# Optimization experiments

Hardware: AMD Instinct MI355X
Metric: run time of the kernel (lower is better)

The kernel has to match this reference:

```python
import jax, jax.numpy as jnp
import numpy as np
from jax import lax

# ---- static config (matches init_kwargs) ----
ORDER = 1
NPTS = ORDER + 1            # 2
JUNC_K = 300
LINE_K = 5000
NMS_SIZE = 3
JUNC_THRESH = 0.008
EPS = 1e-5
B, C, H, W = 4, 256, 160, 160
HID = C // 4                # 64
OUT_CH = [1, 1, 2, 1, 2, 4]  # lmap,jmap,joff,cmap,coff,lvec
NHEADS = len(OUT_CH)
MAXO = max(OUT_CH)          # pad conv2 out-channels to 4 per head
# channel-select indices from padded (NHEADS*MAXO) grouped-conv output
SEL = np.array([h * MAXO + c for h, k in enumerate(OUT_CH) for c in range(k)])
# lvec channel permutation from original forward (identity for order=1)
PERM = np.arange(OUT_CH[-1]).reshape(-1, 2, 2)
PERM[:, 1] = PERM[::-1, 1]
PERM = PERM.reshape(-1)


def setup_inputs() -> dict:
    key = jax.random.key(0)
    ks = jax.random.split(key, 9)
    features = jax.random.normal(ks[0], (B, C, H, W), jnp.float32)
    w1 = jax.random.normal(ks[1], (NHEADS * HID, C, 3, 3), jnp.float32) / np.sqrt(C * 9)
    b1 = 0.01 * jax.random.normal(ks[2], (NHEADS * HID,), jnp.float32)
    gamma = 1.0 + 0.1 * jax.random.normal(ks[3], (NHEADS * HID,), jnp.float32)
    beta = 0.01 * jax.random.normal(ks[4], (NHEADS * HID,), jnp.float32)
    mean = 0.1 * jax.random.normal(ks[5], (NHEADS * HID,), jnp.float32)
    var = jax.random.uniform(ks[6], (NHEADS * HID,), jnp.float32, 0.5, 1.5)
    w2 = jax.random.normal(ks[7], (NHEADS * MAXO, HID, 3, 3), jnp.float32) / np.sqrt(HID * 9)
    b2 = 0.01 * jax.random.normal(ks[8], (NHEADS * MAXO,), jnp.float32)
    return dict(features=features, w1=w1, b1=b1, gamma=gamma, beta=beta,
                mean=mean, var=var, w2=w2, b2=b2)


def _conv(x, w, b, groups=1):
    y = lax.conv_general_dilated(x, w, (1, 1), 'SAME',
                                 dimension_numbers=('NCHW', 'OIHW', 'NCHW'),
                                 feature_group_count=groups)
    return y + b[None, :, None, None]


def _nms(hm):  # hm: (1,H,W) -> suppress non-peaks
    mx = lax.reduce_window(hm, -jnp.inf, lax.max, (1, NMS_SIZE, NMS_SIZE),
                           (1, 1, 1), [(0, 0), (1, 1), (1, 1)])
    return jnp.where(hm == mx, hm, 0.0)


def _post(jm, joff, cm, coff, lv):
    """Per-sample postprocess. jm,cm:(1,H,W) joff,coff:(2,H,W) lv:(4,H,W).
    Returns (pts:(LINE_K,2,2) padded lines, mask:(LINE_K,) validity)."""
    # junctions: NMS + top-K + thresh mask + offset gather
    sj, ij = lax.top_k(_nms(jm).reshape(-1), JUNC_K)
    valid_j = sj >= JUNC_THRESH
    xy = jnp.stack([ij % W, ij // W], -1).astype(jm.dtype)
    junc = xy + joff.reshape(2, -1).T[ij] + 0.5
    junc = jnp.stack([jnp.clip(junc[:, 0], 0.0, W - 1e-4),
                      jnp.clip(junc[:, 1], 0.0, H - 1e-4)], -1)
    # lines: top-K centers + vector field gather (thresh=0 -> always full K)
    sc, ic = lax.top_k(cm.reshape(-1), LINE_K)
    cxy = jnp.stack([ic % W, ic // W], -1).astype(cm.dtype)
    center = cxy + coff.reshape(2, -1).T[ic] + 0.5
    lvr = lv.reshape(NPTS // 2 * 2, 2, -1).transpose(2, 0, 1)  # (HW,2,2)
    loi = center[:, None] + lvr[ic]                            # (L,2,2)
    loi = jnp.stack([jnp.clip(loi[..., 0], 0.0, W - 1e-4),
                     jnp.clip(loi[..., 1], 0.0, H - 1e-4)], -1)
    # pairwise squared-distance argmin of each endpoint to junctions
    d1 = ((loi[:, None, 0] - junc[None]) ** 2).sum(-1)
    d2 = ((loi[:, None, -1] - junc[None]) ** 2).sum(-1)
    big = jnp.asarray(1e18, d1.dtype)
    i1 = jnp.argmin(jnp.where(valid_j[None], d1, big), axis=-1)
    i2 = jnp.argmin(jnp.where(valid_j[None], d2, big), axis=-1)
    imin = jnp.minimum(i1, i2)
    imax = jnp.maximum(i1, i2)
    keep = imin != imax
    # unique (imin,imax) pairs via sorted-key dedup (matches torch.unique order)
    BIGK = JUNC_K * JUNC_K
    keyv = jnp.where(keep, imin * JUNC_K + imax, BIGK)
    sk = jnp.sort(keyv)
    first = jnp.concatenate([jnp.ones((1,), bool), sk[1:] != sk[:-1]]) & (sk < BIGK)
    a = jnp.where(first, sk // JUNC_K, 0)
    b = jnp.where(first, sk % JUNC_K, 0)
    pts = jnp.stack([junc[a], junc[b]], axis=1)  # (L,2,2)
    swap = pts[:, 0, 1] > pts[:, 1, 1]
    pts = jnp.where(swap[:, None, None], pts[:, ::-1], pts)
    return pts, first


def _maps(features, w1, b1, gamma, beta, mean, var, w2, b2):
    y = _conv(features, w1, b1)
    y = (y - mean[None, :, None, None]) * gamma[None, :, None, None] * \
        lax.rsqrt(var + EPS)[None, :, None, None] + beta[None, :, None, None]
    y = jax.nn.relu(y)
    y = _conv(y, w2, b2, groups=NHEADS)        # (B, NHEADS*MAXO, H, W)
    m = y[:, SEL]                              # (B, 11, H, W)
    lmap = jax.nn.sigmoid(m[:, 0:1])
    jmap = jax.nn.sigmoid(m[:, 1:2])
    joff = m[:, 2:4]
    cmap = jax.nn.sigmoid(m[:, 4:5])
    coff = m[:, 5:7]
    lvec = m[:, 7:][:, PERM]
    return lmap, jmap, joff, cmap, coff, lvec


def reference(features, w1, b1, gamma, beta, mean, var, w2, b2):
    lmap, jmap, joff, cmap, coff, lvec = _maps(features, w1, b1, gamma, beta,
                                               mean, var, w2, b2)
    loi, mask = jax.vmap(_post)(jmap, joff, cmap, coff, lvec)
    return lmap, jmap, joff, cmap, coff, lvec, loi, mask


if __name__ == '__main__':
    out = reference(**setup_inputs())
    for o in out:
        print(o.shape, o.dtype)
```

## Files before the change

### kernel.cpp

```cpp
#include <hip/hip_runtime.h>
#include <math.h>

#define IMG   160
#define HWSZ  25600
#define NB    4
#define CIN   256
#define COUT1 384
#define BIGK  90000

#define OFF_LMAP 0
#define OFF_JMAP 102400
#define OFF_JOFF 204800
#define OFF_CMAP 409600
#define OFF_COFF 512000
#define OFF_LVEC 716800
#define OFF_LOI  1126400
#define OFF_MASK 1206400

static const size_t WS_Y1    = 0;
static const size_t WS_JSORT = (size_t)NB * COUT1 * HWSZ * 4;
static const size_t WS_CSORT = WS_JSORT + (size_t)NB * 32768 * 8;
static const size_t WS_JUNC  = WS_CSORT + (size_t)NB * 32768 * 8;
static const size_t WS_JVAL  = WS_JUNC + (size_t)NB * 300 * 2 * 4;
static const size_t WS_LKEY  = WS_JVAL + (size_t)NB * 300 * 4;
static const size_t WS_WPK   = WS_LKEY + (size_t)NB * 8192 * 4;
static const size_t WS_AFTER_WPK = WS_WPK + (size_t)12 * 8 * 9 * 32 * 64 * 2;
static const size_t WS_BNS   = WS_AFTER_WPK;
static const size_t WS_JM    = WS_BNS + 384 * 4;
static const size_t WS_CM    = WS_JM + (size_t)NB * 300 * 8;
static const size_t WS_FPK   = WS_CM + (size_t)NB * 5000 * 8;
static const size_t WS_NEED_MIN = WS_FPK;
static const size_t WS_NEED_PK = WS_FPK + (size_t)NB * 8 * 162 * 162 * 128;

typedef unsigned long long u64;
typedef __attribute__((ext_vector_type(8))) short short8;
typedef __attribute__((ext_vector_type(4))) float f32x4;
typedef __attribute__((ext_vector_type(4))) int int4v;

union frag_u { short8 s8; u64 u[2]; int4v v; };

__device__ __forceinline__ float clip_coord(float v) {
    return fminf(fmaxf(v, 0.0f), 159.9999f);
}
__device__ __forceinline__ float sigmoidf(float v) {
    return 1.0f / (1.0f + expf(-v));
}
__device__ __forceinline__ unsigned short f2bf(float f) {
    unsigned u = __float_as_uint(f);
    return (unsigned short)((u + 0x7FFFu + ((u >> 16) & 1u)) >> 16);
}
__device__ __forceinline__ float bf2f(unsigned short h) {
    return __uint_as_float((unsigned)h << 16);
}

__device__ __forceinline__ void async_copy16(void* lds, const void* g) {
    __builtin_amdgcn_global_load_lds(
        (const __attribute__((address_space(1))) unsigned int*)g,
        (__attribute__((address_space(3))) unsigned int*)lds, 16, 0, 0);
}


__global__ __launch_bounds__(256) void prep_kernel(
    const float* __restrict__ w1, short* __restrict__ wpk,
    const float* __restrict__ gamma, const float* __restrict__ var,
    float* __restrict__ bns,
    const float* __restrict__ feat, short* __restrict__ fpk) {
    const int blk = blockIdx.x;
    const int tid = threadIdx.x;
    if (blk < 6912) {
        int e = blk * 256 + tid;
        int row = e >> 6, sp = e & 63;
        int ocl = row & 31;
        int tap = (row >> 5) % 9;
        int icc = (row / 288) & 7;
        int octile = row / 2304;
        int p16 = sp >> 3, j = sp & 7;
        int l16 = p16 ^ (ocl & 7);
        int ql = l16 * 8 + j;
        int term = ql >> 5, icl = ql & 31;
        int oc = octile * 32 + ocl, ic = icc * 32 + icl;
        float a = w1[((size_t)oc * CIN + ic) * 9 + tap];
        unsigned short hi = f2bf(a);
        wpk[e] = (term == 0) ? (short)hi : (short)f2bf(a - bf2f(hi));
        return;
    }
    if (blk == 6912) {
        for (int i = tid; i < COUT1; i += 256)
            bns[i] = gamma[i] / sqrtf(var[i] + 1e-5f);
        return;
    }
    const int c4  = (tid >> 4) & 3;
    const int r0  = (tid & 15) | (((tid >> 6) & 3) << 4);
    const int rest = (blk - 6913) * 64 + r0;
    const int px = rest % 162;
    const int t2 = rest / 162;
    const int py = t2 % 162;
    const int bi = t2 / 162;
    const int s  = (2 * py + px) & 7;
    const int gy = py - 1, gx = px - 1;
    const bool valid = ((unsigned)gy < (unsigned)IMG) && ((unsigned)gx < (unsigned)IMG);
    const float* fs = feat + (size_t)(bi * 32 + c4 * 8) * HWSZ
                           + (valid ? gy * IMG + gx : 0);
    unsigned hi4[4], lo4[4];
#pragma unroll
    for (int j2 = 0; j2 < 4; ++j2) {
        float va = valid ? fs[(size_t)(2 * j2) * HWSZ]     : 0.0f;
        float vb = valid ? fs[(size_t)(2 * j2 + 1) * HWSZ] : 0.0f;
        unsigned short ha = f2bf(va), hb = f2bf(vb);
        unsigned short la = f2bf(va - bf2f(ha)), lb = f2bf(vb - bf2f(hb));
        hi4[j2] = (unsigned)ha | ((unsigned)hb << 16);
        lo4[j2] = (unsigned)la | ((unsigned)lb << 16);
    }
    const int p0 = c4 ^ s;
    const int p1 = (c4 | 4) ^ s;
    int4v* base = (int4v*)(fpk + (size_t)rest * 64);
    base[p0] = (int4v){ (int)hi4[0], (int)hi4[1], (int)hi4[2], (int)hi4[3] };
    base[p1] = (int4v){ (int)lo4[0], (int)lo4[1], (int)lo4[2], (int)lo4[3] };
}

__global__ __launch_bounds__(512, 2) void conv1_mfma_pk(
    const short* __restrict__ fpk, const short* __restrict__ wpk,
    const float* __restrict__ b1, const float* __restrict__ bns,
    const float* __restrict__ beta, const float* __restrict__ mean,
    float* __restrict__ y1) {
    const int bid   = blockIdx.x;
    const int slot  = bid >> 3;
    const int tile  = (bid & 7) + ((slot / 12) << 3);
    const int octile = slot - (slot / 12) * 12;
    const int bb = tile / 50, tt = tile % 50;
    const int ty = (tt / 5) * 16, tx = (tt % 5) * 32;
    const int oc0 = octile * 32;
    const int tid  = threadIdx.x;
    const int wid  = tid >> 6;
    const int wr   = wid >> 1;
    const int wc   = wid & 1;
    const int lane = tid & 63;
    const int quad = lane >> 4;
    const int l15  = lane & 15;
    const int wbase = tid & ~63;

    __shared__ __align__(16) short Alds[2][288 * 64];
    __shared__ __align__(16) short Blds[612 * 64];

    int aoff[2];
#pragma unroll
    for (int t = 0; t < 2; ++t)
        aoff[t] = l15 * 128 + ((((t << 2) | quad) ^ (l15 & 7)) << 4);

    f32x4 acc[2][4];
#pragma unroll
    for (int mi = 0; mi < 2; ++mi)
#pragma unroll
        for (int nj = 0; nj < 4; ++nj) acc[mi][nj] = (f32x4){0.f, 0.f, 0.f, 0.f};

    const char* asrc0 = (const char*)wpk + (size_t)(octile * 8) * 36864;

    int boff[10];
#pragma unroll
    for (int it = 0; it < 10; ++it) {
        int k = it * 512 + tid;
        int hy = (int)((unsigned)k / 272u);
        int r  = k - hy * 272;
        boff[it] = hy * (162 * 128) + r * 16;
    }
    const char* bsrc0 = (const char*)fpk
        + (((size_t)(bb * 8) * 162 + ty) * 162 + tx) * 128;
    const size_t bstride = (size_t)162 * 162 * 128;

    {
        char* ad = (char*)&Alds[0][0];
#pragma unroll
        for (int i = 0; i < 4; ++i)
            async_copy16(ad + (size_t)(i * 512 + wbase) * 16,
                         asrc0 + (size_t)(i * 512 + tid) * 16);
        if (tid < 256)
            async_copy16(ad + (size_t)(2048 + wbase) * 16,
                         asrc0 + (size_t)(2048 + tid) * 16);
#pragma unroll
        for (int it = 0; it < 9; ++it)
            async_copy16((char*)Blds + (size_t)(it * 512 + wbase) * 16,
                         bsrc0 + boff[it]);
        if (tid < 288) {
            const int4v vv = *(const int4v*)(bsrc0 + boff[9]);
            *(int4v*)((char*)Blds + (size_t)(4608 + tid) * 16) = vv;
        }
    }
    __syncthreads();

    int4v pvB[10];
#pragma unroll 1
    for (int icc = 0; icc < 8; ++icc) {
        const int cur = icc & 1;
        const char* Ab = (const char*)&Alds[cur][0];

        if (icc < 7) {
            const char* as = asrc0 + (size_t)(icc + 1) * 36864;
            char* ad = (char*)&Alds[cur ^ 1][0];
#pragma unroll
            for (int i = 0; i < 4; ++i)
                async_copy16(ad + (size_t)(i * 512 + wbase) * 16,
                             as + (size_t)(i * 512 + tid) * 16);
            if (tid < 256)
                async_copy16(ad + (size_t)(2048 + wbase) * 16,
                             as + (size_t)(2048 + tid) * 16);
            const char* bs = bsrc0 + (size_t)(icc + 1) * bstride;
#pragma unroll
            for (int it = 0; it < 9; ++it)
                pvB[it] = *(const int4v*)(bs + boff[it]);
            if (tid < 288) pvB[9] = *(const int4v*)(bs + boff[9]);
        }

#pragma unroll
        for (int sx = 0; sx < 3; ++sx) {
            frag_u Bf[2][6];
#pragma unroll
            for (int t = 0; t < 2; ++t)
#pragma unroll
                for (int rr = 0; rr < 6; ++rr) {
                    int pos = (wr * 4 + rr) * 34 + (wc * 16 + l15 + sx);
                    const char* bp = (const char*)Blds + (size_t)pos * 128
                        + ((((t << 2) | quad) ^ (pos & 7)) << 4);
                    Bf[t][rr].v = *(const int4v*)bp;
                }
#pragma unroll
            for (int sy = 0; sy < 3; ++sy) {
                const int tap = sy * 3 + sx;
                frag_u Af[2][2];
#pragma unroll
                for (int t = 0; t < 2; ++t)
#pragma unroll
                    for (int mi = 0; mi < 2; ++mi) {
                        const char* ap = Ab
                            + (size_t)(tap * 32 + mi * 16) * 128 + aoff[t];
                        Af[t][mi].v = *(const int4v*)ap;
                    }
#pragma unroll
                for (int mi = 0; mi < 2; ++mi)
#pragma unroll
                    for (int nj = 0; nj < 4; ++nj) {
                        acc[mi][nj] = __builtin_amdgcn_mfma_f32_16x16x32_bf16(
                            Af[0][mi].s8, Bf[0][nj + sy].s8, acc[mi][nj], 0, 0, 0);
                        acc[mi][nj] = __builtin_amdgcn_mfma_f32_16x16x32_bf16(
                            Af[0][mi].s8, Bf[1][nj + sy].s8, acc[mi][nj], 0, 0, 0);
                        acc[mi][nj] = __builtin_amdgcn_mfma_f32_16x16x32_bf16(
                            Af[1][mi].s8, Bf[0][nj + sy].s8, acc[mi][nj], 0, 0, 0);
                    }
            }
        }

        if (icc < 7) {
            __syncthreads();
#pragma unroll
            for (int it = 0; it < 9; ++it)
                *(int4v*)((char*)Blds + (size_t)(it * 512 + tid) * 16) = pvB[it];
            if (tid < 288)
                *(int4v*)((char*)Blds + (size_t)(4608 + tid) * 16) = pvB[9];
            __syncthreads();
        }
    }

#pragma unroll
    for (int nj = 0; nj < 4; ++nj) {
        const int gy = ty + wr * 4 + nj, gx = tx + wc * 16 + l15;
#pragma unroll
        for (int mi = 0; mi < 2; ++mi)
#pragma unroll
            for (int r = 0; r < 4; ++r) {
                const int oc = oc0 + mi * 16 + quad * 4 + r;
                float v = acc[mi][nj][r] + b1[oc];
                v = (v - mean[oc]) * bns[oc] + beta[oc];
                y1[((size_t)(bb * COUT1 + oc)) * HWSZ + gy * IMG + gx] = fmaxf(v, 0.0f);
            }
    }
}


__global__ void wpack_kernel(const float* __restrict__ w1, short* __restrict__ wpk) {
    int e = blockIdx.x * 256 + threadIdx.x;
    int row = e >> 6, sp = e & 63;
    int ocl = row & 31;
    int tap = (row >> 5) % 9;
    int icc = (row / 288) & 7;
    int octile = row / 2304;
    int s = (sp >> 2) ^ (ocl & 15);
    int ql = s * 4 + (sp & 3);
    int term = ql >> 5, icl = ql & 31;
    int oc = octile * 32 + ocl, ic = icc * 32 + icl;
    float a = w1[((size_t)oc * CIN + ic) * 9 + tap];
    unsigned short hi = f2bf(a);
    wpk[e] = (term == 0) ? (short)hi : (short)f2bf(a - bf2f(hi));
}

__global__ __launch_bounds__(256, 2) void conv1_mfma(
    const float* __restrict__ feat, const short* __restrict__ wpk,
    const float* __restrict__ b1, const float* __restrict__ gamma,
    const float* __restrict__ beta, const float* __restrict__ mean,
    const float* __restrict__ var, float* __restrict__ y1) {
    const int bid   = blockIdx.x;
    const int slot  = bid >> 3;
    const int tile  = (bid & 7) + ((slot / 12) << 3);
    const int octile = slot - (slot / 12) * 12;
    const int bb = tile / 100, tt = tile % 100;
    const int ty = (tt / 10) * 16, tx = (tt % 10) * 16;
    const int oc0 = octile * 32;
    const int tid  = threadIdx.x;
    const int w    = tid >> 6;
    const int lane = tid & 63;
    const int quad = lane >> 4;
    const int l15  = lane & 15;

    __shared__ short Alds[288 * 64];
    __shared__ short Blds[324 * 68];

    int aoff[2][2];
#pragma unroll
    for (int t = 0; t < 2; ++t)
#pragma unroll
        for (int h = 0; h < 2; ++h)
            aoff[t][h] = l15 * 128 + (((t * 8 + quad * 2 + h) ^ l15) * 8);

    f32x4 acc[2][4];
#pragma unroll
    for (int mi = 0; mi < 2; ++mi)
#pragma unroll
        for (int nj = 0; nj < 4; ++nj) acc[mi][nj] = (f32x4){0.f, 0.f, 0.f, 0.f};

    const int4v* asrc_base = (const int4v*)wpk + (size_t)(octile * 8) * 2304;
    unsigned* Bd = (unsigned*)Blds;

    float pv0[21], pv1[21];

#pragma unroll
    for (int ii = 0; ii < 21; ++ii) {
        int i = tid + ii * 256;
        if (i < 5184) {
            int icp = i / 324, hp = i - icp * 324;
            int hy = hp / 18, hx = hp - hy * 18;
            int gy = ty + hy - 1, gx = tx + hx - 1;
            bool valid = ((unsigned)gy < IMG) && ((unsigned)gx < IMG);
            const float* fs = feat + ((size_t)(bb * CIN + icp * 2)) * HWSZ
                                   + (valid ? (gy * IMG + gx) : 0);
            pv0[ii] = valid ? fs[0]    : 0.0f;
            pv1[ii] = valid ? fs[HWSZ] : 0.0f;
        }
    }

#pragma unroll 1
    for (int icc = 0; icc < 8; ++icc) {
        __syncthreads();
        {
            const int4v* asrc = asrc_base + (size_t)icc * 2304;
            int4v* adst = (int4v*)Alds;
#pragma unroll
            for (int i = 0; i < 9; ++i)
                adst[tid + i * 256] = asrc[tid + i * 256];
        }
#pragma unroll
        for (int ii = 0; ii < 21; ++ii) {
            int i = tid + ii * 256;
            if (i < 5184) {
                int icp = i / 324, hp = i - icp * 324;
                float v0 = pv0[ii], v1 = pv1[ii];
                unsigned short h0 = f2bf(v0), h1 = f2bf(v1);
                unsigned short m0 = f2bf(v0 - bf2f(h0)), m1 = f2bf(v1 - bf2f(h1));
                Bd[hp * 34 + icp]      = (unsigned)h0 | ((unsigned)h1 << 16);
                Bd[hp * 34 + 16 + icp] = (unsigned)m0 | ((unsigned)m1 << 16);
            }
        }
        __syncthreads();

        if (icc < 7) {
#pragma unroll
            for (int ii = 0; ii < 21; ++ii) {
                int i = tid + ii * 256;
                if (i < 5184) {
                    int icp = i / 324, hp = i - icp * 324;
                    int hy = hp / 18, hx = hp - hy * 18;
                    int gy = ty + hy - 1, gx = tx + hx - 1;
                    bool valid = ((unsigned)gy < IMG) && ((unsigned)gx < IMG);
                    const float* fs = feat
                        + ((size_t)(bb * CIN + (icc + 1) * 32 + icp * 2)) * HWSZ
                        + (valid ? (gy * IMG + gx) : 0);
                    pv0[ii] = valid ? fs[0]    : 0.0f;
                    pv1[ii] = valid ? fs[HWSZ] : 0.0f;
                }
            }
        }

#pragma unroll
        for (int tap = 0; tap < 9; ++tap) {
            const int sy = tap / 3, sx = tap % 3;
            frag_u Af[2][2], Bf[2][4];
#pragma unroll
            for (int t = 0; t < 2; ++t) {
#pragma unroll
                for (int mi = 0; mi < 2; ++mi) {
                    const char* base = (const char*)Alds + (tap * 32 + mi * 16) * 128;
                    Af[t][mi].u[0] = *(const u64*)(base + aoff[t][0]);
                    Af[t][mi].u[1] = *(const u64*)(base + aoff[t][1]);
                }
#pragma unroll
                for (int nj = 0; nj < 4; ++nj) {
                    int pos = (w * 4 + nj + sy) * 18 + (l15 + sx);
                    const short* bp = &Blds[pos * 68 + t * 32 + quad * 8];
                    Bf[t][nj].u[0] = *(const u64*)bp;
                    Bf[t][nj].u[1] = *(const u64*)(bp + 4);
                }
            }
#pragma unroll
            for (int mi = 0; mi < 2; ++mi)
#pragma unroll
                for (int nj = 0; nj < 4; ++nj) {
                    acc[mi][nj] = __builtin_amdgcn_mfma_f32_16x16x32_bf16(
                        Af[0][mi].s8, Bf[0][nj].s8, acc[mi][nj], 0, 0, 0);
                    acc[mi][nj] = __builtin_amdgcn_mfma_f32_16x16x32_bf16(
                        Af[0][mi].s8, Bf[1][nj].s8, acc[mi][nj], 0, 0, 0);
                    acc[mi][nj] = __builtin_amdgcn_mfma_f32_16x16x32_bf16(
                        Af[1][mi].s8, Bf[0][nj].s8, acc[mi][nj], 0, 0, 0);
                    acc[mi][nj] = __builtin_amdgcn_mfma_f32_16x16x32_bf16(
                        Af[1][mi].s8, Bf[1][nj].s8, acc[mi][nj], 0, 0, 0);
                }
        }
    }

#pragma unroll
    for (int nj = 0; nj < 4; ++nj) {
        const int gy = ty + w * 4 + nj, gx = tx + l15;
#pragma unroll
        for (int mi = 0; mi < 2; ++mi)
#pragma unroll
            for (int r = 0; r < 4; ++r) {
                const int oc = oc0 + mi * 16 + quad * 4 + r;
                float v = acc[mi][nj][r] + b1[oc];
                v = (v - mean[oc]) * (gamma[oc] / sqrtf(var[oc] + 1e-5f)) + beta[oc];
                y1[((size_t)(bb * COUT1 + oc)) * HWSZ + gy * IMG + gx] = fmaxf(v, 0.0f);
            }
    }
}


__global__ __launch_bounds__(256, 2) void conv2_kernel(
    const float* __restrict__ y1, const float* __restrict__ w2,
    const float* __restrict__ b2, float* __restrict__ out) {
    const int KH[6]   = {1, 1, 2, 1, 2, 4};
    const int REG[6]  = {OFF_LMAP, OFF_JMAP, OFF_JOFF, OFF_CMAP, OFF_COFF, OFF_LVEC};
    const int SIGF[6] = {1, 1, 0, 1, 0, 0};

    const int bz = blockIdx.z;
    const int b  = bz / 6;
    const int h  = bz % 6;
    const int k  = KH[h];
    const int tx = blockIdx.x * 32, ty = blockIdx.y * 16;
    const int lx = threadIdx.x, ly = threadIdx.y;
    const int tid = ly * 16 + lx;

    __shared__ float tin[16][18][40];
    float* const tinf = &tin[0][0][0];
    float accv[4][2] = {{0.f,0.f},{0.f,0.f},{0.f,0.f},{0.f,0.f}};

    const float* yb = y1 + ((size_t)(b * COUT1 + h * 64)) * HWSZ;

    bool sok[3], sval[3];
    int  soff[3], sidx[3];
#pragma unroll
    for (int j = 0; j < 3; ++j) {
        int idx = tid + j * 256;
        sok[j] = (idx < 612);
        int r = idx / 34, col = idx - r * 34;
        int gy = ty - 1 + r, gx = tx - 1 + col;
        sval[j] = sok[j] && ((unsigned)gy < (unsigned)IMG) && ((unsigned)gx < (unsigned)IMG);
        soff[j] = sval[j] ? (gy * IMG + gx) : 0;
        sidx[j] = r * 40 + col;
    }

    for (int ic0 = 0; ic0 < 64; ic0 += 16) {
        __syncthreads();
#pragma unroll
        for (int j = 0; j < 3; ++j) {
            if (sok[j]) {
                const float* yp = yb + (size_t)ic0 * HWSZ + soff[j];
                float* tp = tinf + sidx[j];
#pragma unroll 4
                for (int c = 0; c < 16; ++c)
                    tp[c * 720] = sval[j] ? yp[(size_t)c * HWSZ] : 0.0f;
            }
        }
        __syncthreads();

        const float* tb = tinf + ly * 40 + 2 * lx;
#pragma unroll 2
        for (int c = 0; c < 16; ++c) {
            const float* tc = tb + c * 720;
            float n[3][4];
#pragma unroll
            for (int r = 0; r < 3; ++r) {
                float2 u = *(const float2*)(tc + r * 40);
                float2 v = *(const float2*)(tc + r * 40 + 2);
                n[r][0] = u.x; n[r][1] = u.y; n[r][2] = v.x; n[r][3] = v.y;
            }
#pragma unroll
            for (int o = 0; o < 4; ++o) {
                if (o < k) {
                    const float* wp = w2 + ((size_t)((h * 4 + o) * 64 + (ic0 + c))) * 9;
                    float a0 = accv[o][0], a1 = accv[o][1];
#pragma unroll
                    for (int r = 0; r < 3; ++r) {
                        float w0 = wp[3*r], w1 = wp[3*r+1], w2v = wp[3*r+2];
                        a0 = fmaf(n[r][0], w0, a0);
                        a1 = fmaf(n[r][1], w0, a1);
                        a0 = fmaf(n[r][1], w1, a0);
                        a1 = fmaf(n[r][2], w1, a1);
                        a0 = fmaf(n[r][2], w2v, a0);
                        a1 = fmaf(n[r][3], w2v, a1);
                    }
                    accv[o][0] = a0; accv[o][1] = a1;
                }
            }
        }
    }

    const int p = (ty + ly) * IMG + tx + 2 * lx;
#pragma unroll
    for (int o = 0; o < 4; ++o) {
        if (o < k) {
            float v0 = accv[o][0] + b2[h * 4 + o];
            float v1 = accv[o][1] + b2[h * 4 + o];
            if (SIGF[h]) { v0 = sigmoidf(v0); v1 = sigmoidf(v1); }
            size_t base = (size_t)REG[h] + ((size_t)(b * k + o)) * HWSZ + p;
            out[base]     = v0;
            out[base + 1] = v1;
        }
    }
}

#define SK64(i) ((i) + ((i) >> 4))
__global__ __launch_bounds__(1024) void sortnms_kernel(
    const float* __restrict__ out, u64* __restrict__ buf) {
    __shared__ u64 s[8192 + 512];
    const int bid = blockIdx.x;
    const int arr = bid >> 2, chunk = bid & 3;
    const bool isj = (arr < 4);
    const int b = arr & 3;
    const float* mp = out + (isj ? OFF_JMAP : OFF_CMAP) + (size_t)b * HWSZ;

    for (int i = threadIdx.x; i < 8192; i += 1024) {
        int p = chunk * 8192 + i;
        u64 key = 0ull;
        if (p < HWSZ) {
            float v = mp[p];
            float nv = v;
            if (isj) {
                const int x = p % IMG, y = p / IMG;
                float mx = v;
#pragma unroll
                for (int dy = -1; dy <= 1; ++dy)
#pragma unroll
                    for (int dx = -1; dx <= 1; ++dx) {
                        int nx = x + dx, ny = y + dy;
                        if (nx >= 0 && nx < IMG && ny >= 0 && ny < IMG)
                            mx = fmaxf(mx, mp[ny * IMG + nx]);
                    }
                nv = (v == mx) ? v : 0.0f;
            }
            key = ((u64)__float_as_uint(nv) << 32)
                | (u64)(0xFFFFFFFFu - (unsigned)p);
        }
        s[SK64(i)] = key;
    }
    for (int k = 2; k <= 8192; k <<= 1)
        for (int j = k >> 1; j > 0; j >>= 1) {
            __syncthreads();
            for (int t = threadIdx.x; t < 4096; t += 1024) {
                int i = ((t & ~(j - 1)) << 1) | (t & (j - 1));
                int l = i | j;
                bool desc = ((i & k) == 0);
                u64 x = s[SK64(i)], y = s[SK64(l)];
                if (desc ? (x < y) : (x > y)) { s[SK64(i)] = y; s[SK64(l)] = x; }
            }
        }
    __syncthreads();
    const size_t base = (size_t)bid * 8192;
    for (int i = threadIdx.x; i < 8192; i += 1024) buf[base + i] = s[SK64(i)];
}

__device__ __forceinline__ int count_gt_desc(const u64* __restrict__ a, u64 e) {
    int cnt = 0;
#pragma unroll
    for (int st = 8192; st > 0; st >>= 1)
        if (cnt + st <= 8192 && a[cnt + st - 1] > e) cnt += st;
    return cnt;
}

__global__ void merge_topk_kernel(const u64* __restrict__ jsort,
                                  const u64* __restrict__ csort,
                                  u64* __restrict__ jm, u64* __restrict__ cm) {
    const int b = blockIdx.y;
    int t = blockIdx.x * 256 + threadIdx.x;
    const u64* src; u64* dst; int K, chunk, pos;
    if (t < 1200) {
        src = jsort + (size_t)b * 32768; dst = jm + (size_t)b * 300;
        K = 300; chunk = t / 300; pos = t - chunk * 300;
    } else {
        t -= 1200;
        if (t >= 20000) return;
        src = csort + (size_t)b * 32768; dst = cm + (size_t)b * 5000;
        K = 5000; chunk = t / 5000; pos = t - chunk * 5000;
    }
    u64 e = src[chunk * 8192 + pos];
    int rank = pos;
#pragma unroll
    for (int c = 0; c < 4; ++c)
        if (c != chunk) rank += count_gt_desc(src + c * 8192, e);
    if (rank < K) dst[rank] = e;
}

__global__ __launch_bounds__(1024) void sort32_lds(int* __restrict__ buf) {
    __shared__ int s[8192];
    int* a = buf + (size_t)blockIdx.x * 8192;
    for (int i = threadIdx.x; i < 8192; i += 1024) s[i] = a[i];
    for (int k = 2; k <= 8192; k <<= 1)
        for (int j = k >> 1; j > 0; j >>= 1) {
            __syncthreads();
            for (int t = threadIdx.x; t < 4096; t += 1024) {
                int i = ((t & ~(j - 1)) << 1) | (t & (j - 1));
                int l = i | j;
                bool asc = ((i & k) == 0);
                int x = s[i], y = s[l];
                if (asc ? (x > y) : (x < y)) { s[i] = y; s[l] = x; }
            }
        }
    __syncthreads();
    for (int i = threadIdx.x; i < 8192; i += 1024) a[i] = s[i];
}

__global__ void lines_kernel(const u64* __restrict__ cmk,
                             const u64* __restrict__ jmk,
                             const float* __restrict__ out,
                             int* __restrict__ lkeys) {
    const int b = blockIdx.y;
    const int t = blockIdx.x * 256 + threadIdx.x;

    __shared__ float jx[300], jy[300];
    __shared__ int jv[300];
    {
        const float* j0 = out + OFF_JOFF + (size_t)(b * 2) * HWSZ;
        const float* j1 = j0 + HWSZ;
        for (int i = threadIdx.x; i < 300; i += 256) {
            u64 key = jmk[(size_t)b * 300 + i];
            float score  = __uint_as_float((unsigned)(key >> 32));
            unsigned idx = 0xFFFFFFFFu - (unsigned)(key & 0xFFFFFFFFull);
            jx[i] = clip_coord((float)(idx % IMG) + j0[idx] + 0.5f);
            jy[i] = clip_coord((float)(idx / IMG) + j1[idx] + 0.5f);
            jv[i] = (score >= 0.008f) ? 1 : 0;
        }
    }
    __syncthreads();

    if (t >= 8192) return;
    if (t >= 5000) { lkeys[b * 8192 + t] = 0x7FFFFFFF; return; }

    u64 key = cmk[(size_t)b * 5000 + t];
    unsigned idx = 0xFFFFFFFFu - (unsigned)(key & 0xFFFFFFFFull);
    const float* c0 = out + OFF_COFF + (size_t)(b * 2) * HWSZ;
    const float* c1 = c0 + HWSZ;
    const float* lv = out + OFF_LVEC + (size_t)(b * 4) * HWSZ;

    float cx = (float)(idx % IMG) + c0[idx] + 0.5f;
    float cy = (float)(idx / IMG) + c1[idx] + 0.5f;
    float e0x = clip_coord(cx + lv[idx]);
    float e0y = clip_coord(cy + lv[HWSZ + idx]);
    float e1x = clip_coord(cx + lv[2 * HWSZ + idx]);
    float e1y = clip_coord(cy + lv[3 * HWSZ + idx]);

    float m1 = 1e18f, m2 = 1e18f;
    int i1 = 0, i2 = 0;
    for (int j = 0; j < 300; ++j) {
        if (jv[j]) {
            float dx = e0x - jx[j], dy = e0y - jy[j];
            float d = dx * dx + dy * dy;
            if (d < m1) { m1 = d; i1 = j; }
            dx = e1x - jx[j]; dy = e1y - jy[j];
            d = dx * dx + dy * dy;
            if (d < m2) { m2 = d; i2 = j; }
        }
    }
    int imin = min(i1, i2), imax = max(i1, i2);
    lkeys[b * 8192 + t] = (i1 != i2) ? (imin * 300 + imax) : BIGK;
}

__global__ void finalize_kernel(const int* __restrict__ lkeys,
                                const u64* __restrict__ jmk,
                                float* __restrict__ out) {
    const int b = blockIdx.y;
    const int t = blockIdx.x * 256 + threadIdx.x;
    if (t >= 5000) return;
    const int* lk = lkeys + b * 8192;
    int sk = lk[t];
    bool first = ((t == 0) || (sk != lk[t - 1])) && (sk < BIGK);
    int a  = first ? sk / 300 : 0;
    int bb = first ? sk % 300 : 0;
    const float* j0 = out + OFF_JOFF + (size_t)(b * 2) * HWSZ;
    const float* j1 = j0 + HWSZ;
    u64 ka = jmk[(size_t)b * 300 + a];
    u64 kb = jmk[(size_t)b * 300 + bb];
    unsigned ia = 0xFFFFFFFFu - (unsigned)(ka & 0xFFFFFFFFull);
    unsigned ib = 0xFFFFFFFFu - (unsigned)(kb & 0xFFFFFFFFull);
    float p0x = clip_coord((float)(ia % IMG) + j0[ia] + 0.5f);
    float p0y = clip_coord((float)(ia / IMG) + j1[ia] + 0.5f);
    float p1x = clip_coord((float)(ib % IMG) + j0[ib] + 0.5f);
    float p1y = clip_coord((float)(ib / IMG) + j1[ib] + 0.5f);
    if (p0y > p1y) {
        float tx = p0x; p0x = p1x; p1x = tx;
        float ty = p0y; p0y = p1y; p1y = ty;
    }
    size_t base = OFF_LOI + (size_t)(b * 5000 + t) * 4;
    out[base]     = p0x;
    out[base + 1] = p0y;
    out[base + 2] = p1x;
    out[base + 3] = p1y;
    out[OFF_MASK + b * 5000 + t] = first ? 1.0f : 0.0f;
}

extern "C" void kernel_launch(void* const* d_in, const int* in_sizes, int n_in,
                              void* d_out, int out_size, void* d_ws, size_t ws_size,
                              hipStream_t stream) {
    const float* feat  = (const float*)d_in[0];
    const float* w1    = (const float*)d_in[1];
    const float* b1    = (const float*)d_in[2];
    const float* gamma = (const float*)d_in[3];
    const float* beta  = (const float*)d_in[4];
    const float* mean  = (const float*)d_in[5];
    const float* var   = (const float*)d_in[6];
    const float* w2    = (const float*)d_in[7];
    const float* b2    = (const float*)d_in[8];
    float* out = (float*)d_out;
    char*  ws  = (char*)d_ws;

    if (ws_size < WS_NEED_MIN) return;

    float* y1 = (float*)(ws + WS_Y1);
    u64* jsort = (u64*)(ws + WS_JSORT);
    int* lkeys  = (int*)(ws + WS_LKEY);
    u64* csort = (u64*)(ws + WS_CSORT);
    short* wpk = (short*)(ws + WS_WPK);
    float* bns = (float*)(ws + WS_BNS);
    u64* jm    = (u64*)(ws + WS_JM);
    u64* cm    = (u64*)(ws + WS_CM);
    short* fpk = (short*)(ws + WS_FPK);

    if (ws_size >= WS_NEED_PK) {
        prep_kernel<<<dim3(20035), dim3(256), 0, stream>>>(
            w1, wpk, gamma, var, bns, feat, fpk);
        conv1_mfma_pk<<<dim3(2400), dim3(512), 0, stream>>>(
            fpk, wpk, b1, bns, beta, mean, y1);
    } else {
        wpack_kernel<<<dim3(6912), dim3(256), 0, stream>>>(w1, wpk);
        conv1_mfma<<<dim3(4800), dim3(256), 0, stream>>>(
            feat, wpk, b1, gamma, beta, mean, var, y1);
    }

    conv2_kernel<<<dim3(5, 10, NB * 6), dim3(16, 16), 0, stream>>>(y1, w2, b2, out);

    sortnms_kernel<<<dim3(32), dim3(1024), 0, stream>>>(out, jsort);

    merge_topk_kernel<<<dim3(83, NB), dim3(256), 0, stream>>>(jsort, csort, jm, cm);

    lines_kernel<<<dim3(32, NB), dim3(256), 0, stream>>>(cm, jm, out, lkeys);

    sort32_lds<<<dim3(NB), dim3(1024), 0, stream>>>(lkeys);

    finalize_kernel<<<dim3(20, NB), dim3(256), 0, stream>>>(lkeys, jm, out);
}
```

Baseline: 1.006 ms.

## Shrink conv1 tiles to 256 threads with single-buffered LDS, fuse sort+finalize

After: 953.2 us (median of 2 runs). 5.2% less time.

```diff
diff --git a/kernel.cpp b/kernel.cpp
--- a/kernel.cpp
+++ b/kernel.cpp
@@ -118,7 +118,7 @@
     base[p1] = (int4v){ (int)lo4[0], (int)lo4[1], (int)lo4[2], (int)lo4[3] };
 }
 
-__global__ __launch_bounds__(512, 2) void conv1_mfma_pk(
+__global__ __launch_bounds__(256, 2) void conv1_mfma_pk(
     const short* __restrict__ fpk, const short* __restrict__ wpk,
     const float* __restrict__ b1, const float* __restrict__ bns,
     const float* __restrict__ beta, const float* __restrict__ mean,
@@ -127,20 +127,18 @@
     const int slot  = bid >> 3;
     const int tile  = (bid & 7) + ((slot / 12) << 3);
     const int octile = slot - (slot / 12) * 12;
-    const int bb = tile / 50, tt = tile % 50;
-    const int ty = (tt / 5) * 16, tx = (tt % 5) * 32;
+    const int bb = tile / 100, tt = tile % 100;
+    const int ty = (tt / 10) * 16, tx = (tt % 10) * 16;
     const int oc0 = octile * 32;
     const int tid  = threadIdx.x;
-    const int wid  = tid >> 6;
-    const int wr   = wid >> 1;
-    const int wc   = wid & 1;
+    const int w    = tid >> 6;
     const int lane = tid & 63;
     const int quad = lane >> 4;
     const int l15  = lane & 15;
-    const int wbase = tid & ~63;
-
-    __shared__ __align__(16) short Alds[2][288 * 64];
-    __shared__ __align__(16) short Blds[612 * 64];
+    const int wbase = tid & 192;
+
+    __shared__ __align__(16) short Alds[288 * 64];
+    __shared__ __align__(16) short Blds[324 * 64];
 
     int aoff[2];
 #pragma unroll
@@ -155,60 +153,36 @@
 
     const char* asrc0 = (const char*)wpk + (size_t)(octile * 8) * 36864;
 
-    int boff[10];
-#pragma unroll
-    for (int it = 0; it < 10; ++it) {
-        int k = it * 512 + tid;
-        int hy = (int)((unsigned)k / 272u);
-        int r  = k - hy * 272;
-        boff[it] = hy * (162 * 128) + r * 16;
-    }
-    const char* bsrc0 = (const char*)fpk
-        + (((size_t)(bb * 8) * 162 + ty) * 162 + tx) * 128;
-    const size_t bstride = (size_t)162 * 162 * 128;
-
-    {
-        char* ad = (char*)&Alds[0][0];
-#pragma unroll
-        for (int i = 0; i < 4; ++i)
-            async_copy16(ad + (size_t)(i * 512 + wbase) * 16,
-                         asrc0 + (size_t)(i * 512 + tid) * 16);
-        if (tid < 256)
-            async_copy16(ad + (size_t)(2048 + wbase) * 16,
-                         asrc0 + (size_t)(2048 + tid) * 16);
-#pragma unroll
-        for (int it = 0; it < 9; ++it)
-            async_copy16((char*)Blds + (size_t)(it * 512 + wbase) * 16,
-                         bsrc0 + boff[it]);
-        if (tid < 288) {
-            const int4v vv = *(const int4v*)(bsrc0 + boff[9]);
-            *(int4v*)((char*)Blds + (size_t)(4608 + tid) * 16) = vv;
-        }
-    }
-    __syncthreads();
-
-    int4v pvB[10];
 #pragma unroll 1
     for (int icc = 0; icc < 8; ++icc) {
-        const int cur = icc & 1;
-        const char* Ab = (const char*)&Alds[cur][0];
-
-        if (icc < 7) {
-            const char* as = asrc0 + (size_t)(icc + 1) * 36864;
-            char* ad = (char*)&Alds[cur ^ 1][0];
-#pragma unroll
-            for (int i = 0; i < 4; ++i)
-                async_copy16(ad + (size_t)(i * 512 + wbase) * 16,
-                             as + (size_t)(i * 512 + tid) * 16);
-            if (tid < 256)
-                async_copy16(ad + (size_t)(2048 + wbase) * 16,
-                             as + (size_t)(2048 + tid) * 16);
-            const char* bs = bsrc0 + (size_t)(icc + 1) * bstride;
-#pragma unroll
-            for (int it = 0; it < 9; ++it)
-                pvB[it] = *(const int4v*)(bs + boff[it]);
-            if (tid < 288) pvB[9] = *(const int4v*)(bs + boff[9]);
-        }
+        __syncthreads();
+        {
+            const char* asrc = asrc0 + (size_t)icc * 36864;
+#pragma unroll
+            for (int i = 0; i < 9; ++i) {
+                int k = i * 256 + tid;
+                async_copy16((char*)Alds + (size_t)(i * 256 + wbase) * 16,
+                             asrc + (size_t)k * 16);
+            }
+        }
+        {
+            const char* bsrc = (const char*)fpk
+                + (((size_t)(bb * 8 + icc) * 162 + ty) * 162 + tx) * 128;
+#pragma unroll
+            for (int it = 0; it < 10; ++it) {
+                int k = it * 256 + tid;
+                int hy = (int)((unsigned)k / 144u);
+                int r  = k - hy * 144;
+                async_copy16((char*)Blds + (size_t)(it * 256 + wbase) * 16,
+                             bsrc + (size_t)hy * (162 * 128) + (size_t)r * 16);
+            }
+            if (tid < 32) {
+                const int4v vv = *(const int4v*)(bsrc + (size_t)17 * (162 * 128)
+                                                 + (size_t)(112 + tid) * 16);
+                *(int4v*)((char*)Blds + (size_t)(2560 + tid) * 16) = vv;
+            }
+        }
+        __syncthreads();
 
 #pragma unroll
         for (int sx = 0; sx < 3; ++sx) {
@@ -217,7 +191,7 @@
             for (int t = 0; t < 2; ++t)
 #pragma unroll
                 for (int rr = 0; rr < 6; ++rr) {
-                    int pos = (wr * 4 + rr) * 34 + (wc * 16 + l15 + sx);
+                    int pos = (w * 4 + rr) * 18 + (l15 + sx);
                     const char* bp = (const char*)Blds + (size_t)pos * 128
                         + ((((t << 2) | quad) ^ (pos & 7)) << 4);
                     Bf[t][rr].v = *(const int4v*)bp;
@@ -230,7 +204,7 @@
                 for (int t = 0; t < 2; ++t)
 #pragma unroll
                     for (int mi = 0; mi < 2; ++mi) {
-                        const char* ap = Ab
+                        const char* ap = (const char*)Alds
                             + (size_t)(tap * 32 + mi * 16) * 128 + aoff[t];
                         Af[t][mi].v = *(const int4v*)ap;
                     }
@@ -247,21 +221,11 @@
                     }
             }
         }
-
-        if (icc < 7) {
-            __syncthreads();
-#pragma unroll
-            for (int it = 0; it < 9; ++it)
-                *(int4v*)((char*)Blds + (size_t)(it * 512 + tid) * 16) = pvB[it];
-            if (tid < 288)
-                *(int4v*)((char*)Blds + (size_t)(4608 + tid) * 16) = pvB[9];
-            __syncthreads();
-        }
     }
 
 #pragma unroll
     for (int nj = 0; nj < 4; ++nj) {
-        const int gy = ty + wr * 4 + nj, gx = tx + wc * 16 + l15;
+        const int gy = ty + w * 4 + nj, gx = tx + l15;
 #pragma unroll
         for (int mi = 0; mi < 2; ++mi)
 #pragma unroll
@@ -614,25 +578,6 @@
     if (rank < K) dst[rank] = e;
 }
 
-__global__ __launch_bounds__(1024) void sort32_lds(int* __restrict__ buf) {
-    __shared__ int s[8192];
-    int* a = buf + (size_t)blockIdx.x * 8192;
-    for (int i = threadIdx.x; i < 8192; i += 1024) s[i] = a[i];
-    for (int k = 2; k <= 8192; k <<= 1)
-        for (int j = k >> 1; j > 0; j >>= 1) {
-            __syncthreads();
-            for (int t = threadIdx.x; t < 4096; t += 1024) {
-                int i = ((t & ~(j - 1)) << 1) | (t & (j - 1));
-                int l = i | j;
-                bool asc = ((i & k) == 0);
-                int x = s[i], y = s[l];
-                if (asc ? (x > y) : (x < y)) { s[i] = y; s[l] = x; }
-            }
-        }
-    __syncthreads();
-    for (int i = threadIdx.x; i < 8192; i += 1024) a[i] = s[i];
-}
-
 __global__ void lines_kernel(const u64* __restrict__ cmk,
                              const u64* __restrict__ jmk,
                              const float* __restrict__ out,
@@ -688,37 +633,52 @@
     lkeys[b * 8192 + t] = (i1 != i2) ? (imin * 300 + imax) : BIGK;
 }
 
-__global__ void finalize_kernel(const int* __restrict__ lkeys,
-                                const u64* __restrict__ jmk,
-                                float* __restrict__ out) {
-    const int b = blockIdx.y;
-    const int t = blockIdx.x * 256 + threadIdx.x;
-    if (t >= 5000) return;
-    const int* lk = lkeys + b * 8192;
-    int sk = lk[t];
-    bool first = ((t == 0) || (sk != lk[t - 1])) && (sk < BIGK);
-    int a  = first ? sk / 300 : 0;
-    int bb = first ? sk % 300 : 0;
+__global__ __launch_bounds__(1024) void sortfin_kernel(
+    const int* __restrict__ lkeys, const u64* __restrict__ jmk,
+    float* __restrict__ out) {
+    __shared__ int s[8192];
+    const int b = blockIdx.x;
+    const int* a = lkeys + (size_t)b * 8192;
+    for (int i = threadIdx.x; i < 8192; i += 1024) s[i] = a[i];
+    for (int k = 2; k <= 8192; k <<= 1)
+        for (int j = k >> 1; j > 0; j >>= 1) {
+            __syncthreads();
+            for (int t = threadIdx.x; t < 4096; t += 1024) {
+                int i = ((t & ~(j - 1)) << 1) | (t & (j - 1));
+                int l = i | j;
+                bool asc = ((i & k) == 0);
+                int x = s[i], y = s[l];
+                if (asc ? (x > y) : (x < y)) { s[i] = y; s[l] = x; }
+            }
+        }
+    __syncthreads();
+
     const float* j0 = out + OFF_JOFF + (size_t)(b * 2) * HWSZ;
     const float* j1 = j0 + HWSZ;
-    u64 ka = jmk[(size_t)b * 300 + a];
-    u64 kb = jmk[(size_t)b * 300 + bb];
-    unsigned ia = 0xFFFFFFFFu - (unsigned)(ka & 0xFFFFFFFFull);
-    unsigned ib = 0xFFFFFFFFu - (unsigned)(kb & 0xFFFFFFFFull);
-    float p0x = clip_coord((float)(ia % IMG) + j0[ia] + 0.5f);
-    float p0y = clip_coord((float)(ia / IMG) + j1[ia] + 0.5f);
-    float p1x = clip_coord((float)(ib % IMG) + j0[ib] + 0.5f);
-    float p1y = clip_coord((float)(ib / IMG) + j1[ib] + 0.5f);
-    if (p0y > p1y) {
-        float tx = p0x; p0x = p1x; p1x = tx;
-        float ty = p0y; p0y = p1y; p1y = ty;
-    }
-    size_t base = OFF_LOI + (size_t)(b * 5000 + t) * 4;
-    out[base]     = p0x;
-    out[base + 1] = p0y;
-    out[base + 2] = p1x;
-    out[base + 3] = p1y;
-    out[OFF_MASK + b * 5000 + t] = first ? 1.0f : 0.0f;
+    for (int t = threadIdx.x; t < 5000; t += 1024) {
+        int sk = s[t];
+        bool first = ((t == 0) || (sk != s[t - 1])) && (sk < BIGK);
+        int aa = first ? sk / 300 : 0;
+        int bb = first ? sk % 300 : 0;
+        u64 ka = jmk[(size_t)b * 300 + aa];
+        u64 kb = jmk[(size_t)b * 300 + bb];
+        unsigned ia = 0xFFFFFFFFu - (unsigned)(ka & 0xFFFFFFFFull);
+        unsigned ib = 0xFFFFFFFFu - (unsigned)(kb & 0xFFFFFFFFull);
+        float p0x = clip_coord((float)(ia % IMG) + j0[ia] + 0.5f);
+        float p0y = clip_coord((float)(ia / IMG) + j1[ia] + 0.5f);
+        float p1x = clip_coord((float)(ib % IMG) + j0[ib] + 0.5f);
+        float p1y = clip_coord((float)(ib / IMG) + j1[ib] + 0.5f);
+        if (p0y > p1y) {
+            float tx = p0x; p0x = p1x; p1x = tx;
+            float ty = p0y; p0y = p1y; p1y = ty;
+        }
+        size_t base = OFF_LOI + (size_t)(b * 5000 + t) * 4;
+        out[base]     = p0x;
+        out[base + 1] = p0y;
+        out[base + 2] = p1x;
+        out[base + 3] = p1y;
+        out[OFF_MASK + b * 5000 + t] = first ? 1.0f : 0.0f;
+    }
 }
 
 extern "C" void kernel_launch(void* const* d_in, const int* in_sizes, int n_in,
@@ -751,7 +711,7 @@
     if (ws_size >= WS_NEED_PK) {
         prep_kernel<<<dim3(20035), dim3(256), 0, stream>>>(
             w1, wpk, gamma, var, bns, feat, fpk);
-        conv1_mfma_pk<<<dim3(2400), dim3(512), 0, stream>>>(
+        conv1_mfma_pk<<<dim3(4800), dim3(256), 0, stream>>>(
             fpk, wpk, b1, bns, beta, mean, y1);
     } else {
         wpack_kernel<<<dim3(6912), dim3(256), 0, stream>>>(w1, wpk);
@@ -767,7 +727,5 @@
 
     lines_kernel<<<dim3(32, NB), dim3(256), 0, stream>>>(cm, jm, out, lkeys);
 
-    sort32_lds<<<dim3(NB), dim3(1024), 0, stream>>>(lkeys);
-
-    finalize_kernel<<<dim3(20, NB), dim3(256), 0, stream>>>(lkeys, jm, out);
-}
+    sortfin_kernel<<<dim3(NB), dim3(1024), 0, stream>>>(lkeys, jm, out);
+}
```
